# Optimization experiments

Hardware: AMD Instinct MI355X
Metric: run time of the kernel (lower is better)

Reference implementation:

```python
import jax, jax.numpy as jnp
import numpy as np

B, T, H, D = 1, 2048, 16, 64
E = H * D          # n_embd = 1024
QKV = 3 * E        # (n_head + 2*n_query_groups) * head_size with groups == heads
DC = 4             # causal conv kernel size (hard-coded d_conv=4)


def setup_inputs() -> dict:
    key = jax.random.key(0)
    ks = jax.random.split(key, 9)
    s = 0.02
    x = jax.random.normal(ks[0], (B, T, E), jnp.float32)
    w_attn = jax.random.normal(ks[1], (E, QKV), jnp.float32) * s
    w_proj = jax.random.normal(ks[2], (E, E), jnp.float32) * s
    qconv_w = jax.random.normal(ks[3], (E, DC), jnp.float32) * 0.3
    kconv_w = jax.random.normal(ks[4], (E, DC), jnp.float32) * 0.3
    vconv_w = jax.random.normal(ks[5], (E, DC), jnp.float32) * 0.3
    # rotate-half RoPE cache, [T, D/2]
    inv_freq = 1.0 / (10000.0 ** (jnp.arange(0, D, 2, dtype=jnp.float32) / D))
    freqs = jnp.outer(jnp.arange(T, dtype=jnp.float32), inv_freq)
    cos, sin = jnp.cos(freqs), jnp.sin(freqs)
    beta = jax.random.uniform(ks[6], (B, T, H), jnp.float32)            # delta-rule write strength in (0,1)
    g = jax.random.uniform(ks[7], (B, T, H), jnp.float32, 0.9, 1.0)     # per-token decay gate in (0.9,1)
    return dict(x=x, w_attn=w_attn, w_proj=w_proj, qconv_w=qconv_w,
                kconv_w=kconv_w, vconv_w=vconv_w, cos=cos, sin=sin,
                beta=beta, g=g)


def causal_conv1d_silu(x, w):
    # x: [B,T,C], w: [C,K] depthwise; left-pad K-1 -> causal, then SiLU.
    C = x.shape[-1]
    xt = jnp.transpose(x, (0, 2, 1))  # [B,C,T]
    y = jax.lax.conv_general_dilated(
        xt, w[:, None, :], (1,), [(DC - 1, 0)],
        dimension_numbers=('NCH', 'OIH', 'NCH'), feature_group_count=C)
    y = jnp.transpose(y, (0, 2, 1))   # [B,T,C]
    return y * jax.nn.sigmoid(y)


def apply_rope(x, cos, sin):
    # x: [B,T,H,D]; rotate-half (interleaved=False) convention.
    x1, x2 = jnp.split(x, 2, axis=-1)
    c = cos[None, :, None, :]
    s = sin[None, :, None, :]
    return jnp.concatenate([x1 * c - x2 * s, x2 * c + x1 * s], axis=-1)


def gated_delta_rule(q, k, v, beta, g):
    # Sequential gated delta-rule recurrence (math equivalent of the chunked kernel).
    # q,k,v: [B,T,H,D]; beta,g: [B,T,H]. State S: [B,H,Dk,Dv].
    scale = 1.0 / jnp.sqrt(jnp.asarray(D, q.dtype))
    qt = jnp.transpose(q, (1, 0, 2, 3))
    kt = jnp.transpose(k, (1, 0, 2, 3))
    vt = jnp.transpose(v, (1, 0, 2, 3))
    bt = jnp.transpose(beta, (1, 0, 2))
    gt = jnp.transpose(g, (1, 0, 2))

    def step(S, inp):
        k_t, v_t, q_t, b_t, g_t = inp
        S = S * g_t[..., None, None]                          # decay
        pred = jnp.einsum('bhk,bhkv->bhv', k_t, S)            # current prediction
        delta = b_t[..., None] * (v_t - pred)                 # delta-rule correction
        S = S + jnp.einsum('bhk,bhv->bhkv', k_t, delta)
        o = jnp.einsum('bhk,bhkv->bhv', q_t, S) * scale
        return S, o

    S0 = jnp.zeros((q.shape[0], H, D, D), q.dtype)
    _, o = jax.lax.scan(step, S0, (kt, vt, qt, bt, gt))
    return jnp.transpose(o, (1, 0, 2, 3))  # [B,T,H,D]


def reference(x, w_attn, w_proj, qconv_w, kconv_w, vconv_w, cos, sin, beta, g):
    Bb, Tt, _ = x.shape
    qkv = x @ w_attn                                   # [B,T,3E]
    qkv = qkv.reshape(Bb, Tt, H, 3, D)                 # q_per_kv=1, total_qkv=3
    q = qkv[:, :, :, 0, :].reshape(Bb, Tt, -1)
    k = qkv[:, :, :, 1, :].reshape(Bb, Tt, -1)
    v = qkv[:, :, :, 2, :].reshape(Bb, Tt, -1)
    # short (causal depthwise) convolutions + SiLU
    q = causal_conv1d_silu(q, qconv_w)
    k = causal_conv1d_silu(k, kconv_w)
    v = causal_conv1d_silu(v, vconv_w)
    q = q.reshape(Bb, Tt, H, D)
    k = k.reshape(Bb, Tt, H, D)
    v = v.reshape(Bb, Tt, H, D)
    q = apply_rope(q, cos, sin)
    k = apply_rope(k, cos, sin)
    # gated delta rule produces the new values fed to attention
    v = gated_delta_rule(q, k, v, beta, g)
    # causal SDPA
    scale = 1.0 / jnp.sqrt(jnp.asarray(D, x.dtype))
    scores = jnp.einsum('bthd,bshd->bhts', q, k) * scale   # [B,H,T,T]
    causal = jnp.tril(jnp.ones((Tt, Tt), bool))
    scores = jnp.where(causal, scores, jnp.asarray(-1e9, scores.dtype))
    attn = jax.nn.softmax(scores, axis=-1)
    y = jnp.einsum('bhts,bshd->bthd', attn, v)
    y = y.reshape(Bb, Tt, -1) @ w_proj
    return y
```

## Files before the change

kernel.cpp:

```cpp
#include <hip/hip_runtime.h>
#include <math.h>

#define TT 2048
#define HH 16
#define DD 64
#define EE 1024
#define NN 3072
#define CHUNK 64
#define NCH (TT / CHUNK)
#define SCALE 0.125f
#define KS 72
#define CPH 8

typedef short bf16x8 __attribute__((ext_vector_type(8)));
typedef short bf16x4 __attribute__((ext_vector_type(4)));
typedef float f32x4 __attribute__((ext_vector_type(4)));
typedef unsigned short ushort;
typedef const __attribute__((address_space(1))) unsigned int* gptr_t;
typedef __attribute__((address_space(3))) unsigned int* lptr_t;

__device__ __forceinline__ unsigned short f2bf(float x) {
    union { float f; unsigned u; } un; un.f = x;
    unsigned r = un.u + 0x7FFFu + ((un.u >> 16) & 1u);
    return (unsigned short)(r >> 16);
}

__device__ __forceinline__ int swz(int r, int c) {
    return (r << 6) + ((((c >> 2) ^ ((r >> 2) & 7)) << 2) | (c & 3));
}
__device__ __forceinline__ int swz4(int r, int c4) {
    return (r << 6) + (((c4 >> 2) ^ ((r >> 2) & 7)) << 2);
}
__device__ __forceinline__ int bswz(int r, int c) {
    return (r << 6) + ((((c >> 3) ^ (r & 7)) << 3) | (c & 7));
}

__global__ __launch_bounds__(256) void cvt_bf16_kernel(
    const float* __restrict__ in, ushort* __restrict__ out)
{
    int i = ((int)blockIdx.x * 256 + (int)threadIdx.x) << 3;
    float4 a = *(const float4*)&in[i];
    float4 b = *(const float4*)&in[i + 4];
    bf16x8 o;
    o[0] = (short)f2bf(a.x); o[1] = (short)f2bf(a.y);
    o[2] = (short)f2bf(a.z); o[3] = (short)f2bf(a.w);
    o[4] = (short)f2bf(b.x); o[5] = (short)f2bf(b.y);
    o[6] = (short)f2bf(b.z); o[7] = (short)f2bf(b.w);
    *(bf16x8*)&out[i] = o;
}

__global__ __launch_bounds__(256) void cvt_transpose_kernel(
    const float* __restrict__ W, ushort* __restrict__ WT, int K, int N)
{
    __shared__ float Ls[64][65];
    int n0 = blockIdx.x * 64, k0 = blockIdx.y * 64;
    int tid = threadIdx.x;
    int lr = tid >> 4, lc4 = (tid & 15) << 2;
    #pragma unroll
    for (int m = 0; m < 4; ++m) {
        int r = lr + m * 16;
        float4 v = *(const float4*)&W[(size_t)(k0 + r) * N + n0 + lc4];
        Ls[r][lc4 + 0] = v.x; Ls[r][lc4 + 1] = v.y;
        Ls[r][lc4 + 2] = v.z; Ls[r][lc4 + 3] = v.w;
    }
    __syncthreads();
    int n = tid >> 2, kb = (tid & 3) << 4;
    bf16x8 o0, o1;
    #pragma unroll
    for (int j = 0; j < 8; ++j) o0[j] = (short)f2bf(Ls[kb + j][n]);
    #pragma unroll
    for (int j = 0; j < 8; ++j) o1[j] = (short)f2bf(Ls[kb + 8 + j][n]);
    *(bf16x8*)&WT[(size_t)(n0 + n) * K + k0 + kb] = o0;
    *(bf16x8*)&WT[(size_t)(n0 + n) * K + k0 + kb + 8] = o1;
}

template<int BM, int BN>
__global__ __launch_bounds__(256) void gemm_bf16(
    const ushort* __restrict__ A, const ushort* __restrict__ BT,
    float* __restrict__ C, int M, int N, int K)
{
    constexpr int MT = BM / 32;
    constexpr int NT = BN / 32;
    constexpr int AIT = BM * 64 / 2048;
    constexpr int BIT = BN * 64 / 2048;
    __shared__ __align__(16) ushort Asl[2][BM * 64];
    __shared__ __align__(16) ushort Bsl[2][BN * 64];
    const int tid = threadIdx.x;
    const int lane = tid & 63, w = tid >> 6;
    const int wm = w >> 1, wn = w & 1;
    const int l16 = lane & 15, lq = lane >> 4;
    const int row0 = blockIdx.y * BM, col0 = blockIdx.x * BN;
    const int wvb = w << 9;

    f32x4 acc[MT][NT];
    #pragma unroll
    for (int i = 0; i < MT; ++i)
        #pragma unroll
        for (int j = 0; j < NT; ++j)
            acc[i][j] = (f32x4){0.f, 0.f, 0.f, 0.f};

#define STAGE_TILE(buf, k0)                                                    \
    {                                                                          \
        _Pragma("unroll")                                                      \
        for (int u = 0; u < AIT; ++u) {                                        \
            int idx = u * 256 + tid;                                           \
            int r = idx >> 3, s = idx & 7;                                     \
            const ushort* srcp =                                               \
                &A[(size_t)(row0 + r) * K + (k0) + ((s ^ (r & 7)) << 3)];      \
            __builtin_amdgcn_global_load_lds((gptr_t)srcp,                     \
                (lptr_t)&Asl[buf][(u << 11) + wvb], 16, 0, 0);                 \
        }                                                                      \
        _Pragma("unroll")                                                      \
        for (int u = 0; u < BIT; ++u) {                                        \
            int idx = u * 256 + tid;                                           \
            int r = idx >> 3, s = idx & 7;                                     \
            const ushort* srcp =                                               \
                &BT[(size_t)(col0 + r) * K + (k0) + ((s ^ (r & 7)) << 3)];     \
            __builtin_amdgcn_global_load_lds((gptr_t)srcp,                     \
                (lptr_t)&Bsl[buf][(u << 11) + wvb], 16, 0, 0);                 \
        }                                                                      \
    }

    const int nK = K >> 6;
    STAGE_TILE(0, 0)
    for (int kt = 0; kt < nK; ++kt) {
        __syncthreads();
        if (kt + 1 < nK) STAGE_TILE((kt + 1) & 1, (kt + 1) << 6)
        const int cb = kt & 1;
        #pragma unroll
        for (int kk = 0; kk < 2; ++kk) {
            bf16x8 afr[MT], bfr[NT];
            #pragma unroll
            for (int mt = 0; mt < MT; ++mt) {
                int rr = wm * (BM / 2) + mt * 16 + l16;
                afr[mt] = *(bf16x8*)&Asl[cb][rr * 64 +
                           (((kk * 4 + lq) ^ (rr & 7)) << 3)];
            }
            #pragma unroll
            for (int nt = 0; nt < NT; ++nt) {
                int cc = wn * (BN / 2) + nt * 16 + l16;
                bfr[nt] = *(bf16x8*)&Bsl[cb][cc * 64 +
                           (((kk * 4 + lq) ^ (cc & 7)) << 3)];
            }
            #pragma unroll
            for (int mt = 0; mt < MT; ++mt)
                #pragma unroll
                for (int nt = 0; nt < NT; ++nt)
                    acc[mt][nt] = __builtin_amdgcn_mfma_f32_16x16x32_bf16(
                        afr[mt], bfr[nt], acc[mt][nt], 0, 0, 0);
        }
    }
#undef STAGE_TILE

    #pragma unroll
    for (int mt = 0; mt < MT; ++mt) {
        #pragma unroll
        for (int nt = 0; nt < NT; ++nt) {
            int col = col0 + wn * (BN / 2) + nt * 16 + l16;
            #pragma unroll
            for (int r = 0; r < 4; ++r) {
                int row = row0 + wm * (BM / 2) + mt * 16 + lq * 4 + r;
                C[(size_t)row * N + col] = acc[mt][nt][r];
            }
        }
    }
}

__global__ __launch_bounds__(256) void conv_rope_kernel(
    const float* __restrict__ qkv,
    const float* __restrict__ qw, const float* __restrict__ kw, const float* __restrict__ vw,
    const float* __restrict__ cosb, const float* __restrict__ sinb,
    float* __restrict__ qo, float* __restrict__ ko, float* __restrict__ vo)
{
    int j = blockIdx.z;
    const float* w = (j == 0) ? qw : (j == 1) ? kw : vw;
    float* dst     = (j == 0) ? qo : (j == 1) ? ko : vo;
    int d  = threadIdx.x;
    int tl = threadIdx.y;
    int t  = blockIdx.x * 4 + tl;
    int h  = blockIdx.y;
    int c  = h * DD + d;
    int n  = h * 192 + j * 64 + d;
    float acc = 0.f;
    #pragma unroll
    for (int i = 0; i < 4; ++i) {
        int tt = t - 3 + i;
        if (tt >= 0) acc = fmaf(qkv[(size_t)tt * NN + n], w[c * 4 + i], acc);
    }
    float yv = acc / (1.f + __expf(-acc));
    if (j == 2) { dst[t * EE + c] = yv; return; }
    __shared__ float sh[4][64];
    sh[tl][d] = yv;
    __syncthreads();
    int dh = d & 31;
    float cc = cosb[t * 32 + dh];
    float ss = sinb[t * 32 + dh];
    float outv;
    if (d < 32) outv = yv * cc - sh[tl][d + 32] * ss;
    else        outv = yv * cc + sh[tl][d - 32] * ss;
    dst[t * EE + c] = outv;
}

__global__ __launch_bounds__(256) void chunk_prep_kernel(
    const float* __restrict__ qb, const float* __restrict__ kb, float* __restrict__ vb,
    const float* __restrict__ beta, const float* __restrict__ g,
    float* __restrict__ Bt, float* __restrict__ Ct, float* __restrict__ Ft)
{
    __shared__ __align__(16) float Kc[4096];
    __shared__ __align__(16) float Vx[4096];
    __shared__ __align__(16) float Mpool[4096];
    __shared__ __align__(16) ushort Abf[4096];
    __shared__ __align__(16) ushort KTb[4096];
    __shared__ __align__(16) ushort XkT[4096];
    __shared__ __align__(16) ushort XvT[4096];
    ushort* Kbf = (ushort*)Mpool;
    ushort* Qbf = (ushort*)Mpool + 4096;
    float*  Mm  = Mpool;

    int c = blockIdx.x, h = blockIdx.y;
    int tid = threadIdx.x;
    int lane = tid & 63;
    int w = tid >> 6;
    int l16 = lane & 15, lq = lane >> 4;
    int t0 = c * CHUNK;

    float gsreg, bsreg;
    {
        float x = g[(t0 + lane) * HH + h];
        #pragma unroll
        for (int off = 1; off < 64; off <<= 1) {
            float y = __shfl_up(x, off);
            if (lane >= off) x *= y;
        }
        gsreg = x;
        bsreg = beta[(t0 + lane) * HH + h];
    }

    {
        int row = tid >> 4, c4 = (tid & 15) << 2;
        #pragma unroll
        for (int m = 0; m < 4; ++m) {
            int r = row + m * 16;
            size_t gidx = (size_t)(t0 + r) * EE + h * DD + c4;
            float4 kv = *(const float4*)&kb[gidx];
            float4 qv = *(const float4*)&qb[gidx];
            float4 vv = *(const float4*)&vb[gidx];
            *(float4*)&Kc[swz4(r, c4)] = kv;
            *(float4*)&Vx[swz4(r, c4)] = vv;
            int ba = bswz(r, c4);
            bf16x4 kb4 = { (short)f2bf(kv.x), (short)f2bf(kv.y),
                           (short)f2bf(kv.z), (short)f2bf(kv.w) };
            bf16x4 qb4 = { (short)f2bf(qv.x), (short)f2bf(qv.y),
                           (short)f2bf(qv.z), (short)f2bf(qv.w) };
            *(bf16x4*)&Kbf[ba] = kb4;
            *(bf16x4*)&Qbf[ba] = qb4;
        }
    }
    __syncthreads();

    f32x4 akk[4], aqk[4];
    {
        bf16x8 kaf[2];
        int rr = w * 16 + l16;
        #pragma unroll
        for (int kk = 0; kk < 2; ++kk)
            kaf[kk] = *(bf16x8*)&Kbf[rr * 64 + (((kk * 4 + lq) ^ (rr & 7)) << 3)];
        #pragma unroll
        for (int ct = 0; ct < 4; ++ct) {
            int tt = ct * 16 + l16;
            f32x4 a1 = {0.f, 0.f, 0.f, 0.f}, a2 = {0.f, 0.f, 0.f, 0.f};
            #pragma unroll
            for (int kk = 0; kk < 2; ++kk) {
                int sl = ((kk * 4 + lq) ^ (tt & 7)) << 3;
                bf16x8 kbfr = *(bf16x8*)&Kbf[tt * 64 + sl];
                bf16x8 qbfr = *(bf16x8*)&Qbf[tt * 64 + sl];
                a1 = __builtin_amdgcn_mfma_f32_16x16x32_bf16(kaf[kk], kbfr, a1, 0, 0, 0);
                a2 = __builtin_amdgcn_mfma_f32_16x16x32_bf16(kaf[kk], qbfr, a2, 0, 0, 0);
            }
            akk[ct] = a1; aqk[ct] = a2;
        }
    }
    __syncthreads();

    {
        int s0 = w * 16 + lq * 4;
        float gS[4];
        #pragma unroll
        for (int r = 0; r < 4; ++r) gS[r] = __shfl(gsreg, s0 + r);
        #pragma unroll
        for (int ct = 0; ct < 4; ++ct) {
            int t = ct * 16 + l16;
            float gT = __shfl(gsreg, t);
            float bT = __shfl(bsreg, t);
            float mw[4];
            bf16x4 ab4;
            #pragma unroll
            for (int r = 0; r < 4; ++r) {
                int s = s0 + r;
                float gr = gT / gS[r];
                mw[r] = bT * gr * akk[ct][r];
                float av = (s <= t) ? SCALE * gr * aqk[ct][r] : 0.f;
                ab4[r] = (short)f2bf(av);
            }
            float4 mw4 = {mw[0], mw[1], mw[2], mw[3]};
            *(float4*)&Mm[swz4(t, s0)] = mw4;
            *(bf16x4*)&Abf[bswz(t, s0)] = ab4;
        }
    }

    {
        float g63 = __shfl(gsreg, 63);
        int s = tid >> 2;
        int cb = (tid & 3) << 4;
        float ratio = g63 / __shfl(gsreg, s);
        #pragma unroll
        for (int u = 0; u < 4; ++u) {
            int b4 = cb + u * 4;
            float4 kv = *(const float4*)&Kc[swz4(s, b4)];
            float kvr[4] = {kv.x, kv.y, kv.z, kv.w};
            #pragma unroll
            for (int j = 0; j < 4; ++j)
                KTb[bswz(b4 + j, s)] = f2bf(ratio * kvr[j]);
        }
    }
    __syncthreads();

    if (tid < 128) {
        int col = tid & 63;
        int wK = tid >> 6;
        float* Xp = wK ? Kc : Vx;
        ushort* XT = wK ? XkT : XvT;
        #pragma unroll 1
        for (int tb = 0; tb < 64; tb += 8) {
            unsigned pk0 = 0, pk1 = 0, pk2 = 0, pk3 = 0;
            #pragma unroll
            for (int u = 0; u < 8; ++u) {
                int t = tb + u;
                float bsv = __shfl(bsreg, t);
                float acc = wK ? (bsv * __shfl(gsreg, t) * Kc[swz(t, col)])
                               : (bsv * Vx[swz(t, col)]);
                int t4 = t & ~3;
                for (int s4 = 0; s4 < t4; s4 += 4) {
                    float4 mp = *(const float4*)&Mm[swz4(t, s4)];
                    acc = fmaf(-mp.x, Xp[swz(s4 + 0, col)], acc);
                    acc = fmaf(-mp.y, Xp[swz(s4 + 1, col)], acc);
                    acc = fmaf(-mp.z, Xp[swz(s4 + 2, col)], acc);
                    acc = fmaf(-mp.w, Xp[swz(s4 + 3, col)], acc);
                }
                for (int s = t4; s < t; ++s)
                    acc = fmaf(-Mm[swz(t, s)], Xp[swz(s, col)], acc);
                Xp[swz(t, col)] = acc;
                unsigned hb = (unsigned)f2bf(acc) << ((u & 1) * 16);
                if (u == 0) pk0 = hb; else if (u == 1) pk0 |= hb;
                else if (u == 2) pk1 = hb; else if (u == 3) pk1 |= hb;
                else if (u == 4) pk2 = hb; else if (u == 5) pk2 |= hb;
                else if (u == 6) pk3 = hb; else pk3 |= hb;
            }
            int slot = (((tb >> 3) ^ (col & 7)) << 3);
            uint4 pkv = {pk0, pk1, pk2, pk3};
            *(uint4*)&XT[col * 64 + slot] = pkv;
        }
    }
    __syncthreads();

    {
        int a_r = w * 16 + l16;
        bf16x8 xkA[2], ktA[2], abA[2];
        #pragma unroll
        for (int kk = 0; kk < 2; ++kk) {
            int sl = ((kk * 4 + lq) ^ (a_r & 7)) << 3;
            xkA[kk] = *(bf16x8*)&XkT[a_r * 64 + sl];
            ktA[kk] = *(bf16x8*)&KTb[a_r * 64 + sl];
            abA[kk] = *(bf16x8*)&Abf[a_r * 64 + sl];
        }
        size_t tile = ((size_t)(c * HH + h)) << 12;
        int a0f = w * 16 + lq * 4;
        #pragma unroll
        for (int ct = 0; ct < 4; ++ct) {
            int b_r = ct * 16 + l16;
            f32x4 accB = {0.f,0.f,0.f,0.f}, accC = {0.f,0.f,0.f,0.f};
            f32x4 accF = {0.f,0.f,0.f,0.f}, accE = {0.f,0.f,0.f,0.f};
            #pragma unroll
            for (int kk = 0; kk < 2; ++kk) {
                int sl = ((kk * 4 + lq) ^ (b_r & 7)) << 3;
                bf16x8 ktB = *(bf16x8*)&KTb[b_r * 64 + sl];
                bf16x8 xvB = *(bf16x8*)&XvT[b_r * 64 + sl];
                bf16x8 abB = *(bf16x8*)&Abf[b_r * 64 + sl];
                accB = __builtin_amdgcn_mfma_f32_16x16x32_bf16(xkA[kk], ktB, accB, 0, 0, 0);
                accC = __builtin_amdgcn_mfma_f32_16x16x32_bf16(ktA[kk], xvB, accC, 0, 0, 0);
                accF = __builtin_amdgcn_mfma_f32_16x16x32_bf16(xkA[kk], abB, accF, 0, 0, 0);
                accE = __builtin_amdgcn_mfma_f32_16x16x32_bf16(abA[kk], xvB, accE, 0, 0, 0);
            }
            float gB = __shfl(gsreg, b_r);
            float4 qv = *(const float4*)&qb[(size_t)(t0 + b_r) * EE + h * DD + a0f];
            float qvr[4] = {qv.x, qv.y, qv.z, qv.w};
            #pragma unroll
            for (int i = 0; i < 4; ++i) {
                int a = a0f + i;
                Bt[tile + (size_t)a * 64 + b_r] = accB[i];
                Ct[tile + (size_t)a * 64 + b_r] = accC[i];
                Ft[tile + (size_t)a * 64 + b_r] = SCALE * gB * qvr[i] - accF[i];
                vb[(size_t)(t0 + a) * EE + h * DD + b_r] = accE[i];
            }
        }
    }
}

__global__ __launch_bounds__(256) void delta_scan4_kernel(
    const float* __restrict__ Bt, const float* __restrict__ Ct,
    const float* __restrict__ g, float* __restrict__ Sout)
{
    __shared__ __align__(16) float Bsb[2][4096];
    __shared__ __align__(16) float Csb[2][512];
    __shared__ float Ss[2][64][10];
    __shared__ float GCs[NCH];
    int bid = (int)blockIdx.x;
    int xcd = bid & 7;
    int idx = bid >> 3;
    int h = xcd + ((idx & 1) << 3);
    int p = idx >> 1;
    int bo = p * 8;
    int tid = threadIdx.x;
    int a = tid & 63;
    int w = tid >> 6;
    int j0 = w * 2;

    {
        float pr = 1.f;
        int t0 = tid * 8;
        #pragma unroll
        for (int j = 0; j < 8; ++j) pr *= g[(t0 + j) * HH + h];
        pr *= __shfl_xor(pr, 1);
        pr *= __shfl_xor(pr, 2);
        pr *= __shfl_xor(pr, 4);
        GCs[tid >> 3] = pr;
        Ss[0][a][j0] = 0.f;
        Ss[0][a][j0 + 1] = 0.f;
    }

#define STG4(buf, cc)                                                          \
    {                                                                          \
        size_t tb = ((size_t)((cc) * HH + h)) << 12;                           \
        _Pragma("unroll")                                                      \
        for (int u = 0; u < 4; ++u) {                                          \
            int fi = ((u << 8) + tid) << 2;                                    \
            int fb = ((u << 8) + (tid & 192)) << 2;                            \
            __builtin_amdgcn_global_load_lds((gptr_t)&Bt[tb + fi],             \
                (lptr_t)&Bsb[buf][fb], 16, 0, 0);                              \
        }                                                                      \
        if (tid < 128) {                                                       \
            size_t cfi = tb + ((size_t)(tid >> 1) << 6) + bo + ((tid & 1) << 2); \
            __builtin_amdgcn_global_load_lds((gptr_t)&Ct[cfi],                 \
                (lptr_t)&Csb[buf][(tid & 64) << 2], 16, 0, 0);                 \
        }                                                                      \
    }

    STG4(0, 0)
    for (int c = 0; c < NCH; ++c) {
        __syncthreads();
        if (c + 1 < NCH) STG4((c + 1) & 1, c + 1)
        const int cb = c & 1;
        const float* Bsp = Bsb[cb];
        const float* Csp = Csb[cb];
        float gc = GCs[c];
        size_t tile = ((size_t)(c * HH + h)) << 12;
        float s0 = Ss[cb][a][j0], s1 = Ss[cb][a][j0 + 1];
        Sout[tile + (size_t)(bo + j0) * 64 + a] = s0;
        Sout[tile + (size_t)(bo + j0 + 1) * 64 + a] = s1;
        float p0 = 0.f, p1 = 0.f;
        #pragma unroll 4
        for (int k = 0; k < 64; ++k) {
            float bk = Bsp[k * 64 + a];
            float2 sv = *(const float2*)&Ss[cb][k][j0];
            p0 = fmaf(bk, sv.x, p0);
            p1 = fmaf(bk, sv.y, p1);
        }
        float c0v = Csp[a * 8 + j0], c1v = Csp[a * 8 + j0 + 1];
        Ss[cb ^ 1][a][j0]     = fmaf(gc, s0, c0v - p0);
        Ss[cb ^ 1][a][j0 + 1] = fmaf(gc, s1, c1v - p1);
    }
#undef STG4
}

__global__ __launch_bounds__(256) void delta_apply_kernel(
    const float* __restrict__ Sb, const float* __restrict__ Ft,
    float* __restrict__ vb)
{
    __shared__ float Fs[64][64];
    __shared__ float S2[64][68];
    int c = blockIdx.x, h = blockIdx.y;
    int tid = threadIdx.x;
    int tx = tid & 15, ty = tid >> 4;
    int a0 = ty << 2, b0 = tx << 2;
    size_t tile = ((size_t)(c * HH + h)) << 12;
    {
        int row = tid >> 4, c4 = (tid & 15) << 2;
        #pragma unroll
        for (int m = 0; m < 4; ++m) {
            int r = row + m * 16;
            *(float4*)&Fs[r][c4] = *(const float4*)&Ft[tile + r * 64 + c4];
            float4 sv = *(const float4*)&Sb[tile + r * 64 + c4];
            S2[c4 + 0][r] = sv.x;
            S2[c4 + 1][r] = sv.y;
            S2[c4 + 2][r] = sv.z;
            S2[c4 + 3][r] = sv.w;
        }
    }
    __syncthreads();
    float accO[4][4] = {};
    #pragma unroll 4
    for (int k = 0; k < 64; ++k) {
        float4 fv = *(const float4*)&Fs[k][a0];
        float4 sv = *(const float4*)&S2[k][b0];
        float fa[4] = {fv.x, fv.y, fv.z, fv.w};
        float sa[4] = {sv.x, sv.y, sv.z, sv.w};
        #pragma unroll
        for (int i = 0; i < 4; ++i)
            #pragma unroll
            for (int j = 0; j < 4; ++j)
                accO[i][j] = fmaf(fa[i], sa[j], accO[i][j]);
    }
    #pragma unroll
    for (int i = 0; i < 4; ++i) {
        size_t gi = (size_t)((c << 6) + a0 + i) * EE + h * DD + b0;
        float4 ev = *(const float4*)&vb[gi];
        float4 ov = {accO[i][0] + ev.x, accO[i][1] + ev.y,
                     accO[i][2] + ev.z, accO[i][3] + ev.w};
        *(float4*)&vb[gi] = ov;
    }
}

__global__ __launch_bounds__(256) void attn_mfma_kernel(
    const float* __restrict__ q, const float* __restrict__ k, const float* __restrict__ v,
    ushort* __restrict__ y)
{
    __shared__ __align__(16) unsigned short KsL[64 * KS];
    __shared__ __align__(16) unsigned short VtL[64 * KS];
    __shared__ __align__(16) unsigned int PL[4][16 * 36];

    int bid = (int)blockIdx.x;
    int xcd = bid & 7;
    int idx = bid >> 3;
    int h = xcd + ((idx & 1) << 3);
    int rb = (31 - (idx >> 1)) * 64;

    int tid = threadIdx.x;
    int w = tid >> 6;
    int lane = tid & 63;
    int l16 = lane & 15;
    int lq = lane >> 4;
    int qr0 = rb + w * 16;
    unsigned* PLw = PL[w];

    bf16x8 qf[2];
    {
        const float* qrow = &q[(size_t)(qr0 + l16) * EE + h * DD];
        #pragma unroll
        for (int kk = 0; kk < 2; ++kk) {
            float4 v0 = *(const float4*)&qrow[kk * 32 + lq * 8];
            float4 v1 = *(const float4*)&qrow[kk * 32 + lq * 8 + 4];
            qf[kk][0] = (short)f2bf(v0.x); qf[kk][1] = (short)f2bf(v0.y);
            qf[kk][2] = (short)f2bf(v0.z); qf[kk][3] = (short)f2bf(v0.w);
            qf[kk][4] = (short)f2bf(v1.x); qf[kk][5] = (short)f2bf(v1.y);
            qf[kk][6] = (short)f2bf(v1.z); qf[kk][7] = (short)f2bf(v1.w);
        }
    }

    f32x4 oacc[4];
    #pragma unroll
    for (int dt = 0; dt < 4; ++dt) oacc[dt] = (f32x4){0.f, 0.f, 0.f, 0.f};
    float mrow = -3e38f, lrow = 0.f;
    const int qrow_i = qr0 + l16;

    int ks_s = tid >> 2, ks_d0 = (tid & 3) << 4;
    int vt_s0 = (tid & 15) << 2;
    int vt_d0 = (tid >> 4) << 2;

    float4 kreg[4];
    f32x4 vreg0, vreg1, vreg2, vreg3;

#define ATT_ISSUE(c0)                                                          \
    {                                                                          \
        const float* krow = &k[(size_t)((c0) + ks_s) * EE + h * DD + ks_d0];   \
        kreg[0] = *(const float4*)&krow[0];                                    \
        kreg[1] = *(const float4*)&krow[4];                                    \
        kreg[2] = *(const float4*)&krow[8];                                    \
        kreg[3] = *(const float4*)&krow[12];                                   \
        const float* vrow = &v[(size_t)((c0) + vt_s0) * EE + h * DD + vt_d0];  \
        vreg0 = *(const f32x4*)&vrow[0];                                       \
        vreg1 = *(const f32x4*)&vrow[EE];                                      \
        vreg2 = *(const f32x4*)&vrow[2 * EE];                                  \
        vreg3 = *(const f32x4*)&vrow[3 * EE];                                  \
    }

    ATT_ISSUE(0)
    for (int c0 = 0; c0 <= rb; c0 += 64) {
        __syncthreads();
        {
            #pragma unroll
            for (int u = 0; u < 4; ++u) {
                bf16x4 pk4 = { (short)f2bf(kreg[u].x), (short)f2bf(kreg[u].y),
                               (short)f2bf(kreg[u].z), (short)f2bf(kreg[u].w) };
                *(bf16x4*)&KsL[ks_s * KS + ks_d0 + u * 4] = pk4;
            }
            #pragma unroll
            for (int dd = 0; dd < 4; ++dd) {
                uint2 pv;
                pv.x = (unsigned)f2bf(vreg0[dd]) | ((unsigned)f2bf(vreg1[dd]) << 16);
                pv.y = (unsigned)f2bf(vreg2[dd]) | ((unsigned)f2bf(vreg3[dd]) << 16);
                *(uint2*)&VtL[(vt_d0 + dd) * KS + vt_s0] = pv;
            }
        }
        __syncthreads();
        if (c0 + 64 <= rb) ATT_ISSUE(c0 + 64)

        f32x4 sacc[4];
        #pragma unroll
        for (int ct = 0; ct < 4; ++ct) {
            bf16x8 ka0 = *(bf16x8*)&KsL[(ct * 16 + l16) * KS + lq * 8];
            bf16x8 ka1 = *(bf16x8*)&KsL[(ct * 16 + l16) * KS + 32 + lq * 8];
            f32x4 acc = {0.f, 0.f, 0.f, 0.f};
            acc = __builtin_amdgcn_mfma_f32_16x16x32_bf16(ka0, qf[0], acc, 0, 0, 0);
            acc = __builtin_amdgcn_mfma_f32_16x16x32_bf16(ka1, qf[1], acc, 0, 0, 0);
            sacc[ct] = acc;
        }

        float sv[4][4];
        float tm = -3e38f;
        #pragma unroll
        for (int ct = 0; ct < 4; ++ct) {
            int sbase = c0 + ct * 16 + lq * 4;
            #pragma unroll
            for (int r = 0; r < 4; ++r) {
                float s = sacc[ct][r] * SCALE;
                if (sbase + r > qrow_i) s = -3e38f;
                sv[ct][r] = s;
                tm = fmaxf(tm, s);
            }
        }
        tm = fmaxf(tm, __shfl_xor(tm, 16));
        tm = fmaxf(tm, __shfl_xor(tm, 32));
        float mn = fmaxf(mrow, tm);
        float corr = __expf(mrow - mn);
        mrow = mn;

        float ps = 0.f;
        #pragma unroll
        for (int ct = 0; ct < 4; ++ct) {
            float p0 = __expf(sv[ct][0] - mn);
            float p1 = __expf(sv[ct][1] - mn);
            float p2 = __expf(sv[ct][2] - mn);
            float p3 = __expf(sv[ct][3] - mn);
            ps += (p0 + p1) + (p2 + p3);
            uint2 wv;
            wv.x = (unsigned)f2bf(p0) | ((unsigned)f2bf(p1) << 16);
            wv.y = (unsigned)f2bf(p2) | ((unsigned)f2bf(p3) << 16);
            *(uint2*)&PLw[l16 * 36 + ct * 8 + lq * 2] = wv;
        }
        ps += __shfl_xor(ps, 16);
        ps += __shfl_xor(ps, 32);
        lrow = lrow * corr + ps;

        float corr_o[4];
        #pragma unroll
        for (int r = 0; r < 4; ++r)
            corr_o[r] = __shfl(corr, (lane & 48) + lq * 4 + r);
        #pragma unroll
        for (int dt = 0; dt < 4; ++dt) {
            #pragma unroll
            for (int r = 0; r < 4; ++r)
                oacc[dt][r] *= corr_o[r];
        }

        bf16x8 pa0 = *(bf16x8*)&PLw[l16 * 36 + lq * 4];
        bf16x8 pa1 = *(bf16x8*)&PLw[l16 * 36 + 16 + lq * 4];
        #pragma unroll
        for (int dt = 0; dt < 4; ++dt) {
            bf16x8 vv0 = *(bf16x8*)&VtL[(dt * 16 + l16) * KS + lq * 8];
            bf16x8 vv1 = *(bf16x8*)&VtL[(dt * 16 + l16) * KS + 32 + lq * 8];
            oacc[dt] = __builtin_amdgcn_mfma_f32_16x16x32_bf16(pa0, vv0, oacc[dt], 0, 0, 0);
            oacc[dt] = __builtin_amdgcn_mfma_f32_16x16x32_bf16(pa1, vv1, oacc[dt], 0, 0, 0);
        }
    }
#undef ATT_ISSUE

    float li = 1.f / lrow;
    float linv_o[4];
    #pragma unroll
    for (int r = 0; r < 4; ++r)
        linv_o[r] = __shfl(li, (lane & 48) + lq * 4 + r);
    #pragma unroll
    for (int dt = 0; dt < 4; ++dt) {
        #pragma unroll
        for (int r = 0; r < 4; ++r) {
            int row = qr0 + lq * 4 + r;
            y[(size_t)row * EE + h * DD + dt * 16 + l16] = f2bf(oacc[dt][r] * linv_o[r]);
        }
    }
}

extern "C" void kernel_launch(void* const* d_in, const int* in_sizes, int n_in,
                              void* d_out, int out_size, void* d_ws, size_t ws_size,
                              hipStream_t stream)
{
    (void)in_sizes; (void)n_in; (void)out_size; (void)ws_size;
    const float* x      = (const float*)d_in[0];
    const float* w_attn = (const float*)d_in[1];
    const float* w_proj = (const float*)d_in[2];
    const float* qcw    = (const float*)d_in[3];
    const float* kcw    = (const float*)d_in[4];
    const float* vcw    = (const float*)d_in[5];
    const float* cosb   = (const float*)d_in[6];
    const float* sinb   = (const float*)d_in[7];
    const float* beta   = (const float*)d_in[8];
    const float* g      = (const float*)d_in[9];
    float* out = (float*)d_out;
    float* ws  = (float*)d_ws;

    const size_t TE = (size_t)TT * EE;
    float* buf0 = ws + 0 * TE;
    float* buf1 = ws + 1 * TE;
    float* buf2 = ws + 2 * TE;
    float* qb   = ws + 3 * TE;
    float* kb   = ws + 4 * TE;
    float* vb   = ws + 5 * TE;
    float* qkv  = buf0;
    ushort* xbf = (ushort*)qb;
    ushort* waT = (ushort*)kb;
    ushort* ybf = (ushort*)buf1;
    ushort* wpT = (ushort*)buf2;
    float* Sbuf = out;

    cvt_bf16_kernel<<<TT * EE / 2048, 256, 0, stream>>>(x, xbf);
    cvt_transpose_kernel<<<dim3(NN / 64, EE / 64), 256, 0, stream>>>(w_attn, waT, EE, NN);
    gemm_bf16<128, 128><<<dim3(NN / 128, TT / 128), 256, 0, stream>>>(
        xbf, waT, qkv, TT, NN, EE);
    conv_rope_kernel<<<dim3(TT / 4, HH, 3), dim3(64, 4), 0, stream>>>(
        qkv, qcw, kcw, vcw, cosb, sinb, qb, kb, vb);
    chunk_prep_kernel<<<dim3(NCH, HH), 256, 0, stream>>>(qb, kb, vb, beta, g, buf0, buf1, buf2);
    delta_scan4_kernel<<<dim3(CPH * HH), 256, 0, stream>>>(buf0, buf1, g, Sbuf);
    delta_apply_kernel<<<dim3(NCH, HH), 256, 0, stream>>>(Sbuf, buf2, vb);
    cvt_transpose_kernel<<<dim3(EE / 64, EE / 64), 256, 0, stream>>>(w_proj, wpT, EE, EE);
    attn_mfma_kernel<<<dim3(512), 256, 0, stream>>>(qb, kb, vb, ybf);
    gemm_bf16<64, 64><<<dim3(EE / 64, TT / 64), 256, 0, stream>>>(
        ybf, wpT, out, TT, EE, EE);
}
```

Measured before the change: 239.8 us.

## Run delta-rule chunk scan on MFMA with split-bf16 precision

The sequential inter-chunk state scan, previously scalar FP32 FMAs over LDS, now uses bf16 MFMA with a hi/lo split (three products) to approximate FP32 accuracy. chunk_prep emits the B matrix as swizzled hi/lo bf16 halves instead of FP32, and each scan block now owns 16 state columns instead of 8, halving the block count. The aim is to shorten the latency-bound serial loop over chunks. The cost is extra precision-splitting work, a dropped lo*lo term, and fewer blocks running in parallel.

```diff
diff --git a/kernel.cpp b/kernel.cpp
--- a/kernel.cpp
+++ b/kernel.cpp
@@ -10,7 +10,7 @@
 #define NCH (TT / CHUNK)
 #define SCALE 0.125f
 #define KS 72
-#define CPH 8
+#define SCPH 4
 
 typedef short bf16x8 __attribute__((ext_vector_type(8)));
 typedef short bf16x4 __attribute__((ext_vector_type(4)));
@@ -23,6 +23,10 @@
     union { float f; unsigned u; } un; un.f = x;
     unsigned r = un.u + 0x7FFFu + ((un.u >> 16) & 1u);
     return (unsigned short)(r >> 16);
+}
+__device__ __forceinline__ float bf2f(unsigned short h) {
+    union { unsigned u; float f; } un; un.u = ((unsigned)h) << 16;
+    return un.f;
 }
 
 __device__ __forceinline__ int swz(int r, int c) {
@@ -204,7 +208,8 @@
 __global__ __launch_bounds__(256) void chunk_prep_kernel(
     const float* __restrict__ qb, const float* __restrict__ kb, float* __restrict__ vb,
     const float* __restrict__ beta, const float* __restrict__ g,
-    float* __restrict__ Bt, float* __restrict__ Ct, float* __restrict__ Ft)
+    ushort* __restrict__ BtTh, ushort* __restrict__ BtTl,
+    float* __restrict__ Ct, float* __restrict__ Ft)
 {
     __shared__ __align__(16) float Kc[4096];
     __shared__ __align__(16) float Vx[4096];
@@ -394,10 +399,21 @@
             float gB = __shfl(gsreg, b_r);
             float4 qv = *(const float4*)&qb[(size_t)(t0 + b_r) * EE + h * DD + a0f];
             float qvr[4] = {qv.x, qv.y, qv.z, qv.w};
+            {
+                bf16x4 hv, lv;
+                #pragma unroll
+                for (int i = 0; i < 4; ++i) {
+                    ushort hb = f2bf(accB[i]);
+                    hv[i] = (short)hb;
+                    lv[i] = (short)f2bf(accB[i] - bf2f(hb));
+                }
+                int sl2 = b_r * 64 + ((((a0f >> 3) ^ (b_r & 7)) << 3) | (a0f & 7));
+                *(bf16x4*)&BtTh[tile + sl2] = hv;
+                *(bf16x4*)&BtTl[tile + sl2] = lv;
+            }
             #pragma unroll
             for (int i = 0; i < 4; ++i) {
                 int a = a0f + i;
-                Bt[tile + (size_t)a * 64 + b_r] = accB[i];
                 Ct[tile + (size_t)a * 64 + b_r] = accC[i];
                 Ft[tile + (size_t)a * 64 + b_r] = SCALE * gB * qvr[i] - accF[i];
                 vb[(size_t)(t0 + a) * EE + h * DD + b_r] = accE[i];
@@ -406,24 +422,27 @@
     }
 }
 
-__global__ __launch_bounds__(256) void delta_scan4_kernel(
-    const float* __restrict__ Bt, const float* __restrict__ Ct,
-    const float* __restrict__ g, float* __restrict__ Sout)
-{
-    __shared__ __align__(16) float Bsb[2][4096];
-    __shared__ __align__(16) float Csb[2][512];
-    __shared__ float Ss[2][64][10];
+__global__ __launch_bounds__(256) void delta_scan5_kernel(
+    const ushort* __restrict__ Bh, const ushort* __restrict__ Bl,
+    const float* __restrict__ Ct, const float* __restrict__ g,
+    float* __restrict__ Sout)
+{
+    __shared__ __align__(16) ushort Bhs[2][4096];
+    __shared__ __align__(16) ushort Bls[2][4096];
+    __shared__ __align__(16) float  Cs[2][1024];
+    __shared__ __align__(16) ushort STh[2][16 * 72];
+    __shared__ __align__(16) ushort STl[2][16 * 72];
     __shared__ float GCs[NCH];
+
     int bid = (int)blockIdx.x;
     int xcd = bid & 7;
     int idx = bid >> 3;
     int h = xcd + ((idx & 1) << 3);
     int p = idx >> 1;
-    int bo = p * 8;
+    int bo = p * 16;
     int tid = threadIdx.x;
-    int a = tid & 63;
-    int w = tid >> 6;
-    int j0 = w * 2;
+    int lane = tid & 63, w = tid >> 6;
+    int l16 = lane & 15, lq = lane >> 4;
 
     {
         float pr = 1.f;
@@ -434,52 +453,70 @@
         pr *= __shfl_xor(pr, 2);
         pr *= __shfl_xor(pr, 4);
         GCs[tid >> 3] = pr;
-        Ss[0][a][j0] = 0.f;
-        Ss[0][a][j0 + 1] = 0.f;
-    }
-
-#define STG4(buf, cc)                                                          \
+    }
+    for (int i = tid; i < 576; i += 256) {
+        ((unsigned*)&STh[0][0])[i] = 0;
+        ((unsigned*)&STl[0][0])[i] = 0;
+    }
+
+#define STG5(buf, cc)                                                          \
     {                                                                          \
         size_t tb = ((size_t)((cc) * HH + h)) << 12;                           \
         _Pragma("unroll")                                                      \
-        for (int u = 0; u < 4; ++u) {                                          \
-            int fi = ((u << 8) + tid) << 2;                                    \
-            int fb = ((u << 8) + (tid & 192)) << 2;                            \
-            __builtin_amdgcn_global_load_lds((gptr_t)&Bt[tb + fi],             \
-                (lptr_t)&Bsb[buf][fb], 16, 0, 0);                              \
+        for (int u = 0; u < 2; ++u) {                                          \
+            int ei = ((u << 8) + tid) << 3;                                    \
+            int eb = ((u << 8) + (tid & 192)) << 3;                            \
+            __builtin_amdgcn_global_load_lds((gptr_t)&Bh[tb + ei],             \
+                (lptr_t)&Bhs[buf][eb], 16, 0, 0);                              \
+            __builtin_amdgcn_global_load_lds((gptr_t)&Bl[tb + ei],             \
+                (lptr_t)&Bls[buf][eb], 16, 0, 0);                              \
         }                                                                      \
-        if (tid < 128) {                                                       \
-            size_t cfi = tb + ((size_t)(tid >> 1) << 6) + bo + ((tid & 1) << 2); \
-            __builtin_amdgcn_global_load_lds((gptr_t)&Ct[cfi],                 \
-                (lptr_t)&Csb[buf][(tid & 64) << 2], 16, 0, 0);                 \
+        {                                                                      \
+            int jq = tid >> 6, aa = tid & 63;                                  \
+            __builtin_amdgcn_global_load_lds(                                  \
+                (gptr_t)&Ct[tb + (size_t)aa * 64 + bo + jq * 4],               \
+                (lptr_t)&Cs[buf][(tid & 192) << 2], 16, 0, 0);                 \
         }                                                                      \
     }
 
-    STG4(0, 0)
+    f32x4 sreg = {0.f, 0.f, 0.f, 0.f};
+    const int ar = w * 16 + l16;
+
+    STG5(0, 0)
     for (int c = 0; c < NCH; ++c) {
         __syncthreads();
-        if (c + 1 < NCH) STG4((c + 1) & 1, c + 1)
+        if (c + 1 < NCH) STG5((c + 1) & 1, c + 1)
         const int cb = c & 1;
-        const float* Bsp = Bsb[cb];
-        const float* Csp = Csb[cb];
         float gc = GCs[c];
         size_t tile = ((size_t)(c * HH + h)) << 12;
-        float s0 = Ss[cb][a][j0], s1 = Ss[cb][a][j0 + 1];
-        Sout[tile + (size_t)(bo + j0) * 64 + a] = s0;
-        Sout[tile + (size_t)(bo + j0 + 1) * 64 + a] = s1;
-        float p0 = 0.f, p1 = 0.f;
-        #pragma unroll 4
-        for (int k = 0; k < 64; ++k) {
-            float bk = Bsp[k * 64 + a];
-            float2 sv = *(const float2*)&Ss[cb][k][j0];
-            p0 = fmaf(bk, sv.x, p0);
-            p1 = fmaf(bk, sv.y, p1);
-        }
-        float c0v = Csp[a * 8 + j0], c1v = Csp[a * 8 + j0 + 1];
-        Ss[cb ^ 1][a][j0]     = fmaf(gc, s0, c0v - p0);
-        Ss[cb ^ 1][a][j0 + 1] = fmaf(gc, s1, c1v - p1);
-    }
-#undef STG4
+        #pragma unroll
+        for (int i = 0; i < 4; ++i)
+            Sout[tile + (size_t)(bo + lq * 4 + i) * 64 + ar] = sreg[i];
+        f32x4 acc = {0.f, 0.f, 0.f, 0.f};
+        #pragma unroll
+        for (int m = 0; m < 2; ++m) {
+            int koff = m * 32 + lq * 8;
+            bf16x8 aHi = *(bf16x8*)&STh[cb][l16 * 72 + koff];
+            bf16x8 aLo = *(bf16x8*)&STl[cb][l16 * 72 + koff];
+            int saddr = ar * 64 + ((((koff >> 3) ^ (ar & 7)) << 3));
+            bf16x8 bHi = *(bf16x8*)&Bhs[cb][saddr];
+            bf16x8 bLo = *(bf16x8*)&Bls[cb][saddr];
+            acc = __builtin_amdgcn_mfma_f32_16x16x32_bf16(aHi, bHi, acc, 0, 0, 0);
+            acc = __builtin_amdgcn_mfma_f32_16x16x32_bf16(aLo, bHi, acc, 0, 0, 0);
+            acc = __builtin_amdgcn_mfma_f32_16x16x32_bf16(aHi, bLo, acc, 0, 0, 0);
+        }
+        f32x4 cvv = *(const f32x4*)&Cs[cb][lq * 256 + ar * 4];
+        #pragma unroll
+        for (int i = 0; i < 4; ++i) {
+            float sn = fmaf(gc, sreg[i], cvv[i] - acc[i]);
+            sreg[i] = sn;
+            ushort hb = f2bf(sn);
+            int j = lq * 4 + i;
+            STh[cb ^ 1][j * 72 + ar] = hb;
+            STl[cb ^ 1][j * 72 + ar] = f2bf(sn - bf2f(hb));
+        }
+    }
+#undef STG5
 }
 
 __global__ __launch_bounds__(256) void delta_apply_kernel(
@@ -729,6 +766,8 @@
     ushort* waT = (ushort*)kb;
     ushort* ybf = (ushort*)buf1;
     ushort* wpT = (ushort*)buf2;
+    ushort* BtTh = (ushort*)buf0;
+    ushort* BtTl = (ushort*)buf0 + 2097152;
     float* Sbuf = out;
 
     cvt_bf16_kernel<<<TT * EE / 2048, 256, 0, stream>>>(x, xbf);
@@ -737,8 +776,9 @@
         xbf, waT, qkv, TT, NN, EE);
     conv_rope_kernel<<<dim3(TT / 4, HH, 3), dim3(64, 4), 0, stream>>>(
         qkv, qcw, kcw, vcw, cosb, sinb, qb, kb, vb);
-    chunk_prep_kernel<<<dim3(NCH, HH), 256, 0, stream>>>(qb, kb, vb, beta, g, buf0, buf1, buf2);
-    delta_scan4_kernel<<<dim3(CPH * HH), 256, 0, stream>>>(buf0, buf1, g, Sbuf);
+    chunk_prep_kernel<<<dim3(NCH, HH), 256, 0, stream>>>(
+        qb, kb, vb, beta, g, BtTh, BtTl, buf1, buf2);
+    delta_scan5_kernel<<<dim3(SCPH * HH), 256, 0, stream>>>(BtTh, BtTl, buf1, g, Sbuf);
     delta_apply_kernel<<<dim3(NCH, HH), 256, 0, stream>>>(Sbuf, buf2, vb);
     cvt_transpose_kernel<<<dim3(EE / 64, EE / 64), 256, 0, stream>>>(w_proj, wpT, EE, EE);
     attn_mfma_kernel<<<dim3(512), 256, 0, stream>>>(qb, kb, vb, ybf);
```

Measured after the change: 216.6 us. -9.7%, faster.
